# Kernel optimization log

Measured on AMD Instinct MI355X. Metric: run time of the kernel, lower is better.

The kernel has to match this reference:

```python
import jax, jax.numpy as jnp
import numpy as np

DN = ('NCHW', 'OIHW', 'NCHW')

def conv3x3(x, w, b):
    y = jax.lax.conv_general_dilated(x, w, window_strides=(1, 1), padding='SAME', dimension_numbers=DN)
    return y + b[None, :, None, None]

def setup_inputs() -> dict:
    key = jax.random.key(0)
    ks = jax.random.split(key, 12)
    B, C, H, W, r = 4, 64, 128, 128, 2
    ic = C * r * r  # 256
    s = 0.02
    inp = {
        'x': jax.random.normal(ks[0], (B, C, H, W), jnp.float32),
        'g_w': jax.random.normal(ks[1], (ic, ic), jnp.float32) * s,
        'g_b': jnp.zeros((ic,), jnp.float32),
        'theta_w': jax.random.normal(ks[2], (ic, ic), jnp.float32) * s,
        'theta_b': jnp.zeros((ic,), jnp.float32),
        'phi_w': jax.random.normal(ks[3], (ic, ic), jnp.float32) * s,
        'phi_b': jnp.zeros((ic,), jnp.float32),
        'Ws_w': jax.random.normal(ks[4], (C, C), jnp.float32) * s,
        'Ws_b': jnp.zeros((C,), jnp.float32),
        'Wc_w': jax.random.normal(ks[5], (C, C), jnp.float32) * s,
        'Wc_b': jnp.zeros((C,), jnp.float32),
        'gamma_s': jnp.ones((1,), jnp.float32),
        'gamma_c': jnp.ones((1,), jnp.float32),
        'm1_w': jax.random.normal(ks[6], (16, C, 3, 3), jnp.float32) * s,
        'm1_b': jnp.zeros((16,), jnp.float32),
        'm2_w': jax.random.normal(ks[7], (1, 16, 3, 3), jnp.float32) * s,
        'm2_b': jnp.zeros((1,), jnp.float32),
    }
    return inp

def reference(x, g_w, g_b, theta_w, theta_b, phi_w, phi_b, Ws_w, Ws_b, Wc_w, Wc_b, gamma_s, gamma_c, m1_w, m1_b, m2_w, m2_b):
    b, c, h, w = x.shape
    ic = g_w.shape[0]
    r = int(round((ic // c) ** 0.5))
    hr, wr = h // r, w // r
    n = hr * wr  # spatial positions after channel-folding
    # x1: [b, ic, n] (row-major reshape, same as torch .reshape)
    x1 = x.reshape(b, ic, n)
    # 1x1 convs == channel matmuls
    g_x = jnp.einsum('oi,bin->bno', g_w, x1) + g_b          # [b, n, ic]
    th = jnp.einsum('oi,bin->bon', theta_w, x1) + theta_b[:, None]  # [b, ic, n]
    ph = jnp.einsum('oi,bin->bon', phi_w, x1) + phi_b[:, None]      # [b, ic, n]
    # spatial attention: [b, n, n]
    f_s = jnp.einsum('bcn,bcm->bnm', th, ph)
    f_s = jax.nn.softmax(f_s, axis=-1)
    y_s = jnp.einsum('bnm,bmo->bno', f_s, g_x)              # [b, n, ic]
    y_s = jnp.transpose(y_s, (0, 2, 1)).reshape(b, c, h, w)
    # channel attention: [b, ic, ic]
    f_c = jnp.einsum('bcn,bdn->bcd', th, ph)
    f_c = jax.nn.softmax(f_c, axis=-1)
    y_c = jnp.einsum('bno,bod->bnd', g_x, f_c).reshape(b, c, h, w)
    ws = jnp.einsum('oi,bihw->bohw', Ws_w, y_s) + Ws_b[None, :, None, None]
    wc = jnp.einsum('oi,bihw->bohw', Wc_w, y_c) + Wc_b[None, :, None, None]
    z = x + gamma_s[0] * ws + gamma_c[0] * wc
    hmid = jax.nn.relu(conv3x3(z, m1_w, m1_b))
    logit = conv3x3(hmid, m2_w, m2_b)
    return (logit, z)
```

## Files before the change

### kernel.cpp

```cpp
#include <hip/hip_runtime.h>
#include <stdint.h>

typedef unsigned short u16;
typedef unsigned int   u32;

typedef __attribute__((ext_vector_type(8)))  short bf16x8;
typedef __attribute__((ext_vector_type(4)))  float f32x4;

__device__ __forceinline__ float b2f(u16 u) { return __uint_as_float(((u32)u) << 16); }
__device__ __forceinline__ float blo(u32 u) { return __uint_as_float(u << 16); }
__device__ __forceinline__ float bhi(u32 u) { return __uint_as_float(u & 0xffff0000u); }
__device__ __forceinline__ u16 f2b(float f) {
    u32 x = __float_as_uint(f);
    u32 r = (x + 0x7fffu + ((x >> 16) & 1u)) >> 16;
    return (u16)r;
}

#define NB   4
#define IC   256
#define NPOS 4096
#define CH   64
#define HW   16384

__global__ __launch_bounds__(256) void prep_kernel(
    const float* __restrict__ wsw, const float* __restrict__ wcw,
    const float* __restrict__ m1w,
    const float* __restrict__ thw, const float* __restrict__ phw, const float* __restrict__ gw,
    float* __restrict__ wswT, float* __restrict__ wcwT, float* __restrict__ m1wT,
    u16* __restrict__ wbf)
{
    int idx = blockIdx.x * 256 + threadIdx.x;
    if (idx < 65536) {
        wbf[idx]          = f2b(thw[idx]);
        wbf[idx + 65536]  = f2b(phw[idx]);
        wbf[idx + 131072] = f2b(gw[idx]);
    }
    if (idx < 4096) {
        int i = idx >> 6, c = idx & 63;
        wswT[i*64 + c] = wsw[c*64 + i];
        wcwT[i*64 + c] = wcw[c*64 + i];
    }
    if (idx < 9216) {
        int o = idx & 15, ct = idx >> 4;
        int t = ct % 9, c = ct / 9;
        m1wT[idx] = m1w[(o*64 + c)*9 + t];
    }
}

__global__ __launch_bounds__(256) void qkv_mfma_kernel(
    const float* __restrict__ x, const u16* __restrict__ wbf,
    const float* __restrict__ thb, const float* __restrict__ phb, const float* __restrict__ gb,
    u16* __restrict__ Q, u16* __restrict__ K, u16* __restrict__ VT)
{
    __shared__ __align__(16) u32 xT[64*132];
    __shared__ __align__(16) float bias_l[256];
    const int tid  = threadIdx.x;
    const int w    = tid >> 6;
    const int lane = tid & 63;
    const int q4   = lane >> 4;
    const int l    = lane & 15;
    const int n0   = blockIdx.x * 64;
    const int b    = blockIdx.y;
    const int mat  = blockIdx.z;
    const u16* wmat = wbf + mat * 65536;
    const float* bias = (mat == 0) ? thb : (mat == 1) ? phb : gb;

    bias_l[tid] = bias[tid];

    {
        const float* xb = x + ((size_t)b*IC)*NPOS + n0;
        int n   = tid & 63;
        int ip0 = tid >> 6;
        #pragma unroll 4
        for (int p=0; p<32; p++){
            int ip = ip0 + p*4;
            float v0 = xb[(size_t)(2*ip  )*NPOS + n];
            float v1 = xb[(size_t)(2*ip+1)*NPOS + n];
            xT[n*132 + ip] = (u32)f2b(v0) | ((u32)f2b(v1) << 16);
        }
    }
    __syncthreads();

    f32x4 acc[4][4];
    #pragma unroll
    for (int ot=0; ot<4; ot++)
        #pragma unroll
        for (int nt=0; nt<4; nt++) acc[ot][nt] = (f32x4){0.f,0.f,0.f,0.f};

    #pragma unroll
    for (int f=0; f<8; f++){
        bf16x8 bfrag[4];
        #pragma unroll
        for (int nt=0; nt<4; nt++)
            bfrag[nt] = *(const bf16x8*)&xT[(nt*16 + l)*132 + f*16 + q4*4];
        #pragma unroll
        for (int ot=0; ot<4; ot++){
            bf16x8 afrag = *(const bf16x8*)(wmat + (size_t)(w*64 + ot*16 + l)*256 + f*32 + q4*8);
            #pragma unroll
            for (int nt=0; nt<4; nt++)
                acc[ot][nt] = __builtin_amdgcn_mfma_f32_16x16x32_bf16(afrag, bfrag[nt], acc[ot][nt], 0, 0, 0);
        }
    }
    __syncthreads();

    if (mat < 2){
        u16* zbuf = (u16*)xT;
        #pragma unroll
        for (int nt=0; nt<4; nt++)
            #pragma unroll
            for (int ot=0; ot<4; ot++){
                int o = w*64 + ot*16 + q4*4;
                float4 bv = *(const float4*)&bias_l[o];
                uint2 pk;
                pk.x = (u32)f2b(acc[ot][nt][0]+bv.x) | ((u32)f2b(acc[ot][nt][1]+bv.y) << 16);
                pk.y = (u32)f2b(acc[ot][nt][2]+bv.z) | ((u32)f2b(acc[ot][nt][3]+bv.w) << 16);
                *(uint2*)&zbuf[(nt*16 + l)*264 + o] = pk;
            }
        __syncthreads();
        u16* dst = ((mat == 0) ? Q : K) + ((size_t)(b*NPOS + n0))*IC;
        int n = tid >> 2, o0 = (tid & 3)*64;
        const u32* src = &xT[n*132 + (tid & 3)*32];
        #pragma unroll
        for (int m=0; m<8; m++)
            *(uint4*)(dst + (size_t)n*IC + o0 + m*8) = ((const uint4*)src)[m];
    } else {
        u16* zbuf = (u16*)xT;
        #pragma unroll
        for (int nt=0; nt<4; nt++)
            #pragma unroll
            for (int ot=0; ot<4; ot++){
                int o = w*64 + ot*16 + q4*4;
                int n = nt*16 + l;
                #pragma unroll
                for (int reg=0; reg<4; reg++)
                    zbuf[(o+reg)*66 + n] = f2b(acc[ot][nt][reg] + bias_l[o+reg]);
            }
        __syncthreads();
        const u32* src = &xT[tid*33];
        u32 tmp[32];
        #pragma unroll
        for (int m=0; m<32; m++) tmp[m] = src[m];
        u16* dst = VT + ((size_t)(b*IC + tid))*NPOS + n0;
        #pragma unroll
        for (int m=0; m<8; m++){
            uint4 v; v.x = tmp[m*4]; v.y = tmp[m*4+1]; v.z = tmp[m*4+2]; v.w = tmp[m*4+3];
            *(uint4*)(dst + m*8) = v;
        }
    }
}

__global__ __launch_bounds__(256) void fc_mfma_kernel(
    const u16* __restrict__ Q, const u16* __restrict__ K, float* __restrict__ fcp)
{
    __shared__ __align__(16) u16 QT[64*72];
    __shared__ __align__(16) u16 KT[64*72];
    const int tid = threadIdx.x;
    const int w   = tid >> 6;
    const int lane = tid & 63;
    const int q4  = lane >> 4;
    const int l   = lane & 15;
    const int c0  = blockIdx.x * 64;
    const int d0  = blockIdx.y * 64;
    const int b   = blockIdx.z >> 2;
    const int nseg= blockIdx.z & 3;

    f32x4 acc[4];
    #pragma unroll
    for (int dt=0; dt<4; dt++) acc[dt] = (f32x4){0.f,0.f,0.f,0.f};

    for (int chunk=0; chunk<16; chunk++){
        const int n0 = nseg*1024 + chunk*64;
        __syncthreads();
        {
            int r  = tid >> 2;
            int cq = (tid & 3) * 16;
            const u16* qs = Q + ((size_t)(b*NPOS + n0 + r))*IC + c0 + cq;
            const u16* ks = K + ((size_t)(b*NPOS + n0 + r))*IC + d0 + cq;
            u16 qv[16], kv[16];
            *(uint4*)&qv[0] = *(const uint4*)qs;
            *(uint4*)&qv[8] = *(const uint4*)(qs + 8);
            *(uint4*)&kv[0] = *(const uint4*)ks;
            *(uint4*)&kv[8] = *(const uint4*)(ks + 8);
            #pragma unroll
            for (int j=0;j<16;j++){
                QT[(cq+j)*72 + r] = qv[j];
                KT[(cq+j)*72 + r] = kv[j];
            }
        }
        __syncthreads();
        #pragma unroll
        for (int f=0; f<2; f++){
            bf16x8 af = *(const bf16x8*)&QT[(w*16 + l)*72 + f*32 + q4*8];
            #pragma unroll
            for (int dt=0; dt<4; dt++){
                bf16x8 bf2 = *(const bf16x8*)&KT[(dt*16 + l)*72 + f*32 + q4*8];
                acc[dt] = __builtin_amdgcn_mfma_f32_16x16x32_bf16(af, bf2, acc[dt], 0, 0, 0);
            }
        }
    }

    #pragma unroll
    for (int dt=0; dt<4; dt++)
        #pragma unroll
        for (int reg=0; reg<4; reg++)
            fcp[((size_t)((nseg*NB + b)*256 + c0 + w*16 + q4*4 + reg))*256 + d0 + dt*16 + l] = acc[dt][reg];
}

__global__ __launch_bounds__(256) void softmax_fc_kernel(
    const float* __restrict__ fcp, float* __restrict__ pc)
{
    __shared__ float red[8];
    const int tid = threadIdx.x;
    const int b = blockIdx.x >> 8, c = blockIdx.x & 255;
    float v = 0.f;
    #pragma unroll
    for (int s=0; s<4; s++)
        v += fcp[((size_t)((s*NB + b)*256 + c))*256 + tid];
    float m = v;
    #pragma unroll
    for (int d=32; d>=1; d>>=1) m = fmaxf(m, __shfl_xor(m, d));
    if ((tid & 63) == 0) red[tid>>6] = m;
    __syncthreads();
    m = fmaxf(fmaxf(red[0],red[1]), fmaxf(red[2],red[3]));
    float e = __expf(v - m);
    float s = e;
    #pragma unroll
    for (int d=32; d>=1; d>>=1) s += __shfl_xor(s, d);
    if ((tid & 63) == 0) red[4 + (tid>>6)] = s;
    __syncthreads();
    s = red[4]+red[5]+red[6]+red[7];
    pc[(size_t)b*65536 + (size_t)c*256 + tid] = e / s;
}

__global__ __launch_bounds__(256) void yc_kernel(
    const u16* __restrict__ VT, const float* __restrict__ pc, u16* __restrict__ ycb)
{
    __shared__ __align__(16) u16 Vt_l[32*64];
    __shared__ __align__(16) float Pt[32*64];
    const int tid = threadIdx.x;
    const int n0 = blockIdx.x * 64, d0 = blockIdx.y * 64, b = blockIdx.z;
    const int tn = tid >> 4, td = tid & 15;
    float acc[4][4];
    #pragma unroll
    for (int j=0;j<4;j++)
        #pragma unroll
        for (int d=0;d<4;d++) acc[j][d]=0.f;
    for (int ot=0; ot<8; ot++){
        int o0 = ot*32;
        __syncthreads();
        {
            int ol = tid >> 3, cc = tid & 7;
            *(uint4*)&Vt_l[ol*64 + cc*8] = *(const uint4*)(VT + ((size_t)(b*IC + o0 + ol))*NPOS + n0 + cc*8);
            const float* ps = pc + (size_t)b*65536 + (size_t)(o0 + ol)*256 + d0 + cc*8;
            *(float4*)&Pt[ol*64 + cc*8]     = *(const float4*)ps;
            *(float4*)&Pt[ol*64 + cc*8 + 4] = *(const float4*)(ps + 4);
        }
        __syncthreads();
        #pragma unroll 4
        for (int kk=0; kk<32; kk++){
            float4 pv = *(const float4*)&Pt[kk*64 + td*4];
            uint2 vp = *(const uint2*)&Vt_l[kk*64 + tn*4];
            float v0 = blo(vp.x), v1 = bhi(vp.x), v2 = blo(vp.y), v3 = bhi(vp.y);
            acc[0][0] = fmaf(v0, pv.x, acc[0][0]); acc[0][1] = fmaf(v0, pv.y, acc[0][1]);
            acc[0][2] = fmaf(v0, pv.z, acc[0][2]); acc[0][3] = fmaf(v0, pv.w, acc[0][3]);
            acc[1][0] = fmaf(v1, pv.x, acc[1][0]); acc[1][1] = fmaf(v1, pv.y, acc[1][1]);
            acc[1][2] = fmaf(v1, pv.z, acc[1][2]); acc[1][3] = fmaf(v1, pv.w, acc[1][3]);
            acc[2][0] = fmaf(v2, pv.x, acc[2][0]); acc[2][1] = fmaf(v2, pv.y, acc[2][1]);
            acc[2][2] = fmaf(v2, pv.z, acc[2][2]); acc[2][3] = fmaf(v2, pv.w, acc[2][3]);
            acc[3][0] = fmaf(v3, pv.x, acc[3][0]); acc[3][1] = fmaf(v3, pv.y, acc[3][1]);
            acc[3][2] = fmaf(v3, pv.z, acc[3][2]); acc[3][3] = fmaf(v3, pv.w, acc[3][3]);
        }
    }
    #pragma unroll
    for (int j=0;j<4;j++){
        u32 lo = (u32)f2b(acc[j][0]) | ((u32)f2b(acc[j][1]) << 16);
        u32 hi = (u32)f2b(acc[j][2]) | ((u32)f2b(acc[j][3]) << 16);
        *(uint2*)&ycb[((size_t)b*NPOS + n0 + tn*4 + j)*IC + d0 + td*4] = make_uint2(lo,hi);
    }
}

__global__ __launch_bounds__(256) void flash_mfma_kernel(
    const u16* __restrict__ Q, const u16* __restrict__ K, const u16* __restrict__ VT,
    u16* __restrict__ opart0, u16* __restrict__ opartx, float* __restrict__ lpart,
    int sshift)
{
    __shared__ __align__(16) u32 Kt[8192];
    __shared__ __align__(16) u32 Vt[8192];
    __shared__ __align__(16) u16 Pl[4608];
    const int tid  = threadIdx.x;
    const int w    = tid >> 6;
    const int lane = tid & 63;
    const int q4   = lane >> 4;
    const int l    = lane & 15;
    const int S    = 1 << sshift;
    const int b    = blockIdx.y >> sshift;
    const int seg  = blockIdx.y & (S - 1);
    const int n0   = blockIdx.x * 64;
    const int tiles = 64 >> sshift;
    const int kt0   = seg * tiles;

    bf16x8 qf[8];
    {
        const u16* qrow = Q + ((size_t)(b*NPOS + n0 + w*16 + l))*IC;
        #pragma unroll
        for (int f=0; f<8; f++)
            qf[f] = *(const bf16x8*)(qrow + f*32 + q4*8);
    }

    f32x4 oacc[16];
    #pragma unroll
    for (int t=0;t<16;t++) oacc[t] = (f32x4){0.f,0.f,0.f,0.f};
    float lrow[4] = {0.f, 0.f, 0.f, 0.f};

    u16* Pz = Pl + w*1152;

    auto stage_k = [&](int m0s){
        #pragma unroll
        for (int j=0;j<8;j++){
            int call = w*8 + j;
            int r = call*2 + (lane>>5);
            int c = (lane & 31) ^ (r & 7);
            const u16* g = K + ((size_t)(b*NPOS + m0s + r))*IC + c*8;
            __builtin_amdgcn_global_load_lds(
                (const __attribute__((address_space(1))) u32*)(const void*)g,
                (__attribute__((address_space(3))) u32*)(void*)&Kt[call*256], 16, 0, 0);
        }
    };
    auto stage_v = [&](int m0s){
        #pragma unroll
        for (int j=0;j<8;j++){
            int call = w*8 + j;
            int d = call*8 + (lane>>3);
            int c = (lane & 7) ^ (d & 7);
            const u16* g = VT + ((size_t)(b*IC + d))*NPOS + m0s + c*8;
            __builtin_amdgcn_global_load_lds(
                (const __attribute__((address_space(1))) u32*)(const void*)g,
                (__attribute__((address_space(3))) u32*)(void*)&Vt[call*256], 16, 0, 0);
        }
    };

    stage_k(kt0*64);
    stage_v(kt0*64);
    asm volatile("s_waitcnt vmcnt(0)" ::: "memory");
    __builtin_amdgcn_sched_barrier(0);
    __builtin_amdgcn_s_barrier();
    __builtin_amdgcn_sched_barrier(0);

    for (int kti=0; kti<tiles; kti++){
        const bool more = (kti + 1 < tiles);
        const int mn = (kt0 + kti + 1)*64;

        f32x4 sac[4];
        #pragma unroll
        for (int t=0;t<4;t++) sac[t] = (f32x4){0.f,0.f,0.f,0.f};
        __builtin_amdgcn_s_setprio(1);
        #pragma unroll
        for (int f=0; f<8; f++){
            #pragma unroll
            for (int t=0;t<4;t++){
                int r = t*16 + l;
                int c = (f*4 + q4) ^ (r & 7);
                bf16x8 kf = *(const bf16x8*)((const u16*)Kt + r*256 + c*8);
                sac[t] = __builtin_amdgcn_mfma_f32_16x16x32_bf16(qf[f], kf, sac[t], 0, 0, 0);
            }
        }
        __builtin_amdgcn_s_setprio(0);

        __builtin_amdgcn_sched_barrier(0);
        __builtin_amdgcn_s_barrier();
        __builtin_amdgcn_sched_barrier(0);

        if (more) stage_k(mn);

        #pragma unroll
        for (int reg=0; reg<4; reg++){
            float p0 = __expf(sac[0][reg]), p1 = __expf(sac[1][reg]);
            float p2 = __expf(sac[2][reg]), p3 = __expf(sac[3][reg]);
            lrow[reg] += (p0+p1) + (p2+p3);
            int m = q4*4 + reg;
            Pz[m*72 + l]      = f2b(p0);
            Pz[m*72 + 16 + l] = f2b(p1);
            Pz[m*72 + 32 + l] = f2b(p2);
            Pz[m*72 + 48 + l] = f2b(p3);
        }

        if (more) { asm volatile("s_waitcnt vmcnt(8)" ::: "memory"); }
        else      { asm volatile("s_waitcnt vmcnt(0)" ::: "memory"); }
        __builtin_amdgcn_sched_barrier(0);
        __builtin_amdgcn_s_barrier();
        __builtin_amdgcn_sched_barrier(0);

        __builtin_amdgcn_s_setprio(1);
        #pragma unroll
        for (int s2=0; s2<2; s2++){
            bf16x8 pa = *(const bf16x8*)(Pz + l*72 + s2*32 + q4*8);
            #pragma unroll
            for (int t=0;t<16;t++){
                int d = t*16 + l;
                int c = (s2*4 + q4) ^ (d & 7);
                bf16x8 vb = *(const bf16x8*)((const u16*)Vt + d*64 + c*8);
                oacc[t] = __builtin_amdgcn_mfma_f32_16x16x32_bf16(pa, vb, oacc[t], 0, 0, 0);
            }
        }
        __builtin_amdgcn_s_setprio(0);

        __builtin_amdgcn_sched_barrier(0);
        __builtin_amdgcn_s_barrier();
        __builtin_amdgcn_sched_barrier(0);

        if (more) {
            stage_v(mn);
            asm volatile("s_waitcnt vmcnt(8)" ::: "memory");
        } else {
            asm volatile("s_waitcnt vmcnt(0)" ::: "memory");
        }
        __builtin_amdgcn_sched_barrier(0);
        __builtin_amdgcn_s_barrier();
        __builtin_amdgcn_sched_barrier(0);
    }

    #pragma unroll
    for (int reg=0; reg<4; reg++){
        float v = lrow[reg];
        v += __shfl_xor(v, 1); v += __shfl_xor(v, 2);
        v += __shfl_xor(v, 4); v += __shfl_xor(v, 8);
        if (l == 0)
            lpart[((size_t)(seg*NB + b))*NPOS + n0 + w*16 + q4*4 + reg] = v;
    }

    __syncthreads();
    u16* Ez = (u16*)Kt + w*4096;
    #pragma unroll
    for (int t=0;t<16;t++)
        #pragma unroll
        for (int reg=0;reg<4;reg++)
            Ez[(t*16 + l)*16 + q4*4 + reg] = f2b(oacc[t][reg]);
    u16* base = (seg == 0) ? opart0 : (opartx + (size_t)(seg-1)*((size_t)NB*IC*NPOS));
    u16* dst = base + (size_t)b*(IC*NPOS) + n0 + w*16;
    for (int p=0; p<32; p++){
        int d = p*8 + (lane>>3);
        u32 val = *(const u32*)(Ez + d*16 + (lane&7)*2);
        *(u32*)(dst + (size_t)d*NPOS + (lane&7)*2) = val;
    }
}

__global__ __launch_bounds__(256) void combine_kernel(
    u16* __restrict__ opart0, const u16* __restrict__ opartx,
    const float* __restrict__ lpart, int S)
{
    const int idx = blockIdx.x * 256 + threadIdx.x;
    const int b   = idx >> 17;
    const int rem = idx & 131071;
    const int o   = rem >> 9;
    const int n   = (rem & 511) * 8;
    const size_t base = ((size_t)b*IC + o)*NPOS + n;
    float acc[8] = {0,0,0,0,0,0,0,0};
    float L[8]   = {0,0,0,0,0,0,0,0};
    for (int s=0; s<S; s++){
        const u16* p = (s == 0) ? opart0 : (opartx + (size_t)(s-1)*((size_t)NB*IC*NPOS));
        uint4 v = *(const uint4*)(p + base);
        acc[0] += blo(v.x); acc[1] += bhi(v.x);
        acc[2] += blo(v.y); acc[3] += bhi(v.y);
        acc[4] += blo(v.z); acc[5] += bhi(v.z);
        acc[6] += blo(v.w); acc[7] += bhi(v.w);
        const float* lp = lpart + ((size_t)(s*NB + b))*NPOS + n;
        float4 l0 = *(const float4*)lp;
        float4 l1 = *(const float4*)(lp + 4);
        L[0]+=l0.x; L[1]+=l0.y; L[2]+=l0.z; L[3]+=l0.w;
        L[4]+=l1.x; L[5]+=l1.y; L[6]+=l1.z; L[7]+=l1.w;
    }
    uint4 out;
    out.x = (u32)f2b(acc[0]/L[0]) | ((u32)f2b(acc[1]/L[1]) << 16);
    out.y = (u32)f2b(acc[2]/L[2]) | ((u32)f2b(acc[3]/L[3]) << 16);
    out.z = (u32)f2b(acc[4]/L[4]) | ((u32)f2b(acc[5]/L[5]) << 16);
    out.w = (u32)f2b(acc[6]/L[6]) | ((u32)f2b(acc[7]/L[7]) << 16);
    *(uint4*)(opart0 + base) = out;
}

__global__ __launch_bounds__(256) void z_kernel(
    const float* __restrict__ x, const u16* __restrict__ ysT, const u16* __restrict__ ycb,
    const float* __restrict__ wswT, const float* __restrict__ wcwT,
    const float* __restrict__ wsb, const float* __restrict__ wcb,
    const float* __restrict__ gs, const float* __restrict__ gc,
    float* __restrict__ zout)
{
    __shared__ __align__(16) float Wsl[64*32];
    __shared__ __align__(16) float Wcl[64*32];
    const int tid = threadIdx.x;
    const int p = blockIdx.x * 256 + tid;
    const int cbase = blockIdx.y * 32;
    const int b = blockIdx.z;
    {
        int i = tid >> 2, c8 = (tid & 3) * 8;
        const float* s1 = wswT + i*64 + cbase + c8;
        const float* s2 = wcwT + i*64 + cbase + c8;
        *(float4*)&Wsl[i*32 + c8]     = *(const float4*)s1;
        *(float4*)&Wsl[i*32 + c8 + 4] = *(const float4*)(s1+4);
        *(float4*)&Wcl[i*32 + c8]     = *(const float4*)s2;
        *(float4*)&Wcl[i*32 + c8 + 4] = *(const float4*)(s2+4);
    }
    __syncthreads();
    float as[32], ac[32];
    #pragma unroll
    for (int c=0;c<32;c++){ as[c]=0.f; ac[c]=0.f; }
    const u16* ysp = ysT + (size_t)b*(IC*NPOS) + p;
    const u16* ycp = ycb + (size_t)b*(IC*NPOS) + p;
    for (int i=0;i<64;i++){
        float ysv = b2f(ysp[(size_t)i*HW]);
        float ycv = b2f(ycp[(size_t)i*HW]);
        #pragma unroll
        for (int c=0;c<32;c++){
            as[c] = fmaf(Wsl[i*32+c], ysv, as[c]);
            ac[c] = fmaf(Wcl[i*32+c], ycv, ac[c]);
        }
    }
    float gsv = gs[0], gcv = gc[0];
    #pragma unroll
    for (int c=0;c<32;c++){
        int cg = cbase + c;
        float xv = x[((size_t)b*CH + cg)*HW + p];
        float zv = fmaf(gsv, as[c] + wsb[cg], xv);
        zv = fmaf(gcv, ac[c] + wcb[cg], zv);
        zout[((size_t)b*CH + cg)*HW + p] = zv;
    }
}

__global__ __launch_bounds__(256) void conv1_kernel(
    const float* __restrict__ z, const float* __restrict__ m1wT, const float* __restrict__ m1b,
    float* __restrict__ hmid)
{
    const int tid = threadIdx.x;
    const int p = blockIdx.x * 128 + (tid & 127);
    const int oh = (tid >> 7) * 8;
    const int b = blockIdx.y;
    const int y = p >> 7, xx = p & 127;
    float acc[8];
    #pragma unroll
    for (int o=0;o<8;o++) acc[o]=0.f;
    for (int c=0;c<64;c++){
        const float* zp = z + ((size_t)b*CH + c)*HW;
        #pragma unroll
        for (int t=0;t<9;t++){
            int dy = t/3 - 1, dx = t%3 - 1;
            int yy = y + dy, xv = xx + dx;
            float zv = 0.f;
            if (yy >= 0 && yy < 128 && xv >= 0 && xv < 128) zv = zp[yy*128 + xv];
            const float* w = m1wT + (c*9 + t)*16 + oh;
            #pragma unroll
            for (int o=0;o<8;o++) acc[o] = fmaf(w[o], zv, acc[o]);
        }
    }
    #pragma unroll
    for (int o=0;o<8;o++)
        hmid[((size_t)b*16 + oh + o)*HW + p] = fmaxf(acc[o] + m1b[oh + o], 0.f);
}

__global__ __launch_bounds__(256) void conv2_kernel(
    const float* __restrict__ hmid, const float* __restrict__ m2w, const float* __restrict__ m2b,
    float* __restrict__ logit)
{
    const int idx = blockIdx.x * 256 + threadIdx.x;
    const int b = idx >> 14, p = idx & 16383;
    const int y = p >> 7, xx = p & 127;
    float acc = 0.f;
    for (int c=0;c<16;c++){
        const float* hp = hmid + ((size_t)b*16 + c)*HW;
        #pragma unroll
        for (int t=0;t<9;t++){
            int dy = t/3 - 1, dx = t%3 - 1;
            int yy = y + dy, xv = xx + dx;
            if (yy >= 0 && yy < 128 && xv >= 0 && xv < 128)
                acc = fmaf(m2w[c*9+t], hp[yy*128 + xv], acc);
        }
    }
    logit[idx] = acc + m2b[0];
}

extern "C" void kernel_launch(void* const* d_in, const int* in_sizes, int n_in,
                              void* d_out, int out_size, void* d_ws, size_t ws_size,
                              hipStream_t stream)
{
    const float* x    = (const float*)d_in[0];
    const float* g_w  = (const float*)d_in[1];
    const float* g_b  = (const float*)d_in[2];
    const float* th_w = (const float*)d_in[3];
    const float* th_b = (const float*)d_in[4];
    const float* ph_w = (const float*)d_in[5];
    const float* ph_b = (const float*)d_in[6];
    const float* ws_w = (const float*)d_in[7];
    const float* ws_b = (const float*)d_in[8];
    const float* wc_w = (const float*)d_in[9];
    const float* wc_b = (const float*)d_in[10];
    const float* gs   = (const float*)d_in[11];
    const float* gc   = (const float*)d_in[12];
    const float* m1w  = (const float*)d_in[13];
    const float* m1b  = (const float*)d_in[14];
    const float* m2w  = (const float*)d_in[15];
    const float* m2b  = (const float*)d_in[16];

    char* ws = (char*)d_ws;
    u16*   Qb   = (u16*)  (ws + 0);
    u16*   Kb   = (u16*)  (ws + 8388608);
    u16*   VTb  = (u16*)  (ws + 16777216);
    u16*   ysT  = (u16*)  (ws + 25165824);
    u16*   ycb  = (u16*)  (ws + 33554432);
    u16*   wbf  = (u16*)  (ws + 41943040);
    float* pc   = (float*)(ws + 42991616);
    float* fcp  = (float*)(ws + 44040192);
    float* hmid = (float*)(ws + 44040192);
    float* lpart= (float*)(ws + 44040192);
    float* wswT = (float*)(ws + 48234496);
    float* wcwT = (float*)(ws + 48250880);
    float* m1wT = (float*)(ws + 48267264);
    u16*   opartx = (u16*)(ws + 48304128);

    float* logit = (float*)d_out;
    float* zout  = (float*)d_out + 65536;

    int sshift = 0;
    if (ws_size >= 48304128ULL + 3ULL*8388608ULL)      sshift = 2;
    else if (ws_size >= 48304128ULL + 1ULL*8388608ULL) sshift = 1;

    prep_kernel<<<256, 256, 0, stream>>>(ws_w, wc_w, m1w, th_w, ph_w, g_w,
                                         wswT, wcwT, m1wT, wbf);
    qkv_mfma_kernel<<<dim3(64,4,3), 256, 0, stream>>>(x, wbf, th_b, ph_b, g_b, Qb, Kb, VTb);
    fc_mfma_kernel<<<dim3(4,4,16), 256, 0, stream>>>(Qb, Kb, fcp);
    softmax_fc_kernel<<<1024, 256, 0, stream>>>(fcp, pc);
    yc_kernel<<<dim3(64,4,4), 256, 0, stream>>>(VTb, pc, ycb);
    flash_mfma_kernel<<<dim3(64, NB << sshift), 256, 0, stream>>>(Qb, Kb, VTb, ysT, opartx, lpart, sshift);
    combine_kernel<<<2048, 256, 0, stream>>>(ysT, opartx, lpart, 1 << sshift);
    z_kernel<<<dim3(64,2,4), 256, 0, stream>>>(x, ysT, ycb, wswT, wcwT, ws_b, wc_b, gs, gc, zout);
    conv1_kernel<<<dim3(128,4), 256, 0, stream>>>(zout, m1wT, m1b, hmid);
    conv2_kernel<<<256, 256, 0, stream>>>(hmid, m2w, m2b, logit);
}
```

Before: 459.4 us.

## Switch flash attention kernel to 32x32x16 MFMA with 2x2 wave tiling

Restructures the flash attention kernel to use 32x32x16 bf16 MFMA instructions. The four waves now form a 2x2 grid over query rows and key columns instead of each wave owning 16 query rows across all keys. Each wave computes its partial QK^T split across two accumulators, writes exponentials into a shared swizzled P tile, and computes a quarter of the output channels. The row-sum reduction across the key halves goes through LDS. It also sets launch_bounds to 2 blocks per CU. The aim is fewer, larger MFMAs and fewer LDS fragment reads per FLOP, at the cost of more register pressure and an extra cross-wave sum.

```diff
diff --git a/kernel.cpp b/kernel.cpp
--- a/kernel.cpp
+++ b/kernel.cpp
@@ -6,6 +6,7 @@
 
 typedef __attribute__((ext_vector_type(8)))  short bf16x8;
 typedef __attribute__((ext_vector_type(4)))  float f32x4;
+typedef __attribute__((ext_vector_type(16))) float f32x16;
 
 __device__ __forceinline__ float b2f(u16 u) { return __uint_as_float(((u32)u) << 16); }
 __device__ __forceinline__ float blo(u32 u) { return __uint_as_float(u << 16); }
@@ -279,40 +280,45 @@
     }
 }
 
-__global__ __launch_bounds__(256) void flash_mfma_kernel(
+__global__ __launch_bounds__(256, 2) void flash_mfma_kernel(
     const u16* __restrict__ Q, const u16* __restrict__ K, const u16* __restrict__ VT,
     u16* __restrict__ opart0, u16* __restrict__ opartx, float* __restrict__ lpart,
     int sshift)
 {
     __shared__ __align__(16) u32 Kt[8192];
     __shared__ __align__(16) u32 Vt[8192];
-    __shared__ __align__(16) u16 Pl[4608];
+    __shared__ __align__(16) u16 Pl[4096];
     const int tid  = threadIdx.x;
     const int w    = tid >> 6;
     const int lane = tid & 63;
-    const int q4   = lane >> 4;
-    const int l    = lane & 15;
+    const int l31  = lane & 31;
+    const int hi   = lane >> 5;
+    const int wq   = w >> 1;
+    const int wk   = w & 1;
     const int S    = 1 << sshift;
     const int b    = blockIdx.y >> sshift;
     const int seg  = blockIdx.y & (S - 1);
     const int n0   = blockIdx.x * 64;
     const int tiles = 64 >> sshift;
     const int kt0   = seg * tiles;
-
-    bf16x8 qf[8];
+    const int sw    = l31 & 7;
+
+    bf16x8 qf[16];
     {
-        const u16* qrow = Q + ((size_t)(b*NPOS + n0 + w*16 + l))*IC;
-        #pragma unroll
-        for (int f=0; f<8; f++)
-            qf[f] = *(const bf16x8*)(qrow + f*32 + q4*8);
-    }
-
-    f32x4 oacc[16];
-    #pragma unroll
-    for (int t=0;t<16;t++) oacc[t] = (f32x4){0.f,0.f,0.f,0.f};
-    float lrow[4] = {0.f, 0.f, 0.f, 0.f};
-
-    u16* Pz = Pl + w*1152;
+        const u16* qrow = Q + ((size_t)(b*NPOS + n0 + wq*32 + l31))*IC;
+        #pragma unroll
+        for (int st=0; st<16; st++)
+            qf[st] = *(const bf16x8*)(qrow + st*16 + hi*8);
+    }
+
+    f32x16 oacc[4];
+    #pragma unroll
+    for (int t=0;t<4;t++)
+        #pragma unroll
+        for (int i=0;i<16;i++) oacc[t][i] = 0.f;
+    float lsum[16];
+    #pragma unroll
+    for (int i=0;i<16;i++) lsum[i] = 0.f;
 
     auto stage_k = [&](int m0s){
         #pragma unroll
@@ -346,60 +352,56 @@
     __builtin_amdgcn_s_barrier();
     __builtin_amdgcn_sched_barrier(0);
 
+    const u16* KtRow = (const u16*)Kt + (wk*32 + l31)*256;
+    const u16* PlRow = Pl + (wq*32 + l31)*64;
+    const u16* VtW   = (const u16*)Vt + (wk*128 + l31)*64;
+
     for (int kti=0; kti<tiles; kti++){
         const bool more = (kti + 1 < tiles);
         const int mn = (kt0 + kti + 1)*64;
 
-        f32x4 sac[4];
-        #pragma unroll
-        for (int t=0;t<4;t++) sac[t] = (f32x4){0.f,0.f,0.f,0.f};
+        f32x16 sA, sB;
+        #pragma unroll
+        for (int i=0;i<16;i++){ sA[i]=0.f; sB[i]=0.f; }
         __builtin_amdgcn_s_setprio(1);
         #pragma unroll
-        for (int f=0; f<8; f++){
+        for (int st=0; st<8; st++){
+            bf16x8 ka = *(const bf16x8*)(KtRow + ((st*2+hi) ^ sw)*8);
+            sA = __builtin_amdgcn_mfma_f32_32x32x16_bf16(qf[st], ka, sA, 0, 0, 0);
+            bf16x8 kb = *(const bf16x8*)(KtRow + (((st+8)*2+hi) ^ sw)*8);
+            sB = __builtin_amdgcn_mfma_f32_32x32x16_bf16(qf[st+8], kb, sB, 0, 0, 0);
+        }
+        __builtin_amdgcn_s_setprio(0);
+
+        #pragma unroll
+        for (int reg=0; reg<16; reg++){
+            float p = __expf(sA[reg] + sB[reg]);
+            lsum[reg] += p;
+            int q = wq*32 + (reg&3) + 8*(reg>>2) + 4*hi;
+            int cpos = (((wk*4 + (l31>>3)) ^ (q&7)) * 8) + (lane & 7);
+            Pl[q*64 + cpos] = f2b(p);
+        }
+
+        __builtin_amdgcn_sched_barrier(0);
+        __builtin_amdgcn_s_barrier();
+        __builtin_amdgcn_sched_barrier(0);
+
+        if (more) stage_k(mn);
+
+        if (more) { asm volatile("s_waitcnt vmcnt(8) lgkmcnt(0)" ::: "memory"); }
+        else      { asm volatile("s_waitcnt vmcnt(0) lgkmcnt(0)" ::: "memory"); }
+        __builtin_amdgcn_sched_barrier(0);
+        __builtin_amdgcn_s_barrier();
+        __builtin_amdgcn_sched_barrier(0);
+
+        __builtin_amdgcn_s_setprio(1);
+        #pragma unroll
+        for (int ks=0; ks<4; ks++){
+            bf16x8 pa = *(const bf16x8*)(PlRow + ((ks*2+hi) ^ sw)*8);
             #pragma unroll
-            for (int t=0;t<4;t++){
-                int r = t*16 + l;
-                int c = (f*4 + q4) ^ (r & 7);
-                bf16x8 kf = *(const bf16x8*)((const u16*)Kt + r*256 + c*8);
-                sac[t] = __builtin_amdgcn_mfma_f32_16x16x32_bf16(qf[f], kf, sac[t], 0, 0, 0);
-            }
-        }
-        __builtin_amdgcn_s_setprio(0);
-
-        __builtin_amdgcn_sched_barrier(0);
-        __builtin_amdgcn_s_barrier();
-        __builtin_amdgcn_sched_barrier(0);
-
-        if (more) stage_k(mn);
-
-        #pragma unroll
-        for (int reg=0; reg<4; reg++){
-            float p0 = __expf(sac[0][reg]), p1 = __expf(sac[1][reg]);
-            float p2 = __expf(sac[2][reg]), p3 = __expf(sac[3][reg]);
-            lrow[reg] += (p0+p1) + (p2+p3);
-            int m = q4*4 + reg;
-            Pz[m*72 + l]      = f2b(p0);
-            Pz[m*72 + 16 + l] = f2b(p1);
-            Pz[m*72 + 32 + l] = f2b(p2);
-            Pz[m*72 + 48 + l] = f2b(p3);
-        }
-
-        if (more) { asm volatile("s_waitcnt vmcnt(8)" ::: "memory"); }
-        else      { asm volatile("s_waitcnt vmcnt(0)" ::: "memory"); }
-        __builtin_amdgcn_sched_barrier(0);
-        __builtin_amdgcn_s_barrier();
-        __builtin_amdgcn_sched_barrier(0);
-
-        __builtin_amdgcn_s_setprio(1);
-        #pragma unroll
-        for (int s2=0; s2<2; s2++){
-            bf16x8 pa = *(const bf16x8*)(Pz + l*72 + s2*32 + q4*8);
-            #pragma unroll
-            for (int t=0;t<16;t++){
-                int d = t*16 + l;
-                int c = (s2*4 + q4) ^ (d & 7);
-                bf16x8 vb = *(const bf16x8*)((const u16*)Vt + d*64 + c*8);
-                oacc[t] = __builtin_amdgcn_mfma_f32_16x16x32_bf16(pa, vb, oacc[t], 0, 0, 0);
+            for (int dt=0; dt<4; dt++){
+                bf16x8 vb = *(const bf16x8*)(VtW + dt*2048 + ((ks*2+hi) ^ sw)*8);
+                oacc[dt] = __builtin_amdgcn_mfma_f32_32x32x16_bf16(pa, vb, oacc[dt], 0, 0, 0);
             }
         }
         __builtin_amdgcn_s_setprio(0);
@@ -419,28 +421,52 @@
         __builtin_amdgcn_sched_barrier(0);
     }
 
-    #pragma unroll
-    for (int reg=0; reg<4; reg++){
-        float v = lrow[reg];
-        v += __shfl_xor(v, 1); v += __shfl_xor(v, 2);
-        v += __shfl_xor(v, 4); v += __shfl_xor(v, 8);
-        if (l == 0)
-            lpart[((size_t)(seg*NB + b))*NPOS + n0 + w*16 + q4*4 + reg] = v;
-    }
-
+    float lv[16];
+    #pragma unroll
+    for (int reg=0; reg<16; reg++){
+        float v = lsum[reg];
+        v += __shfl_xor(v, 1); v += __shfl_xor(v, 2); v += __shfl_xor(v, 4);
+        v += __shfl_xor(v, 8); v += __shfl_xor(v, 16);
+        lv[reg] = v;
+    }
+    float* lred = (float*)Pl;
+    if (wk == 1 && l31 == 0){
+        #pragma unroll
+        for (int reg=0; reg<16; reg++)
+            lred[wq*32 + (reg&3) + 8*(reg>>2) + 4*hi] = lv[reg];
+    }
+
+    u16* LDSO = (u16*)Kt;
+    #pragma unroll
+    for (int dt=0; dt<4; dt++){
+        int d = wk*128 + dt*32 + l31;
+        int dsw = d & 15;
+        #pragma unroll
+        for (int pr=0; pr<8; pr++){
+            int r0 = pr*2;
+            int n = wq*32 + (r0&3) + 8*(r0>>2) + 4*hi;
+            u32 pk = (u32)f2b(oacc[dt][r0]) | ((u32)f2b(oacc[dt][r0+1]) << 16);
+            *(u32*)&LDSO[d*64 + (((n>>1) ^ dsw) * 2)] = pk;
+        }
+    }
     __syncthreads();
-    u16* Ez = (u16*)Kt + w*4096;
-    #pragma unroll
-    for (int t=0;t<16;t++)
-        #pragma unroll
-        for (int reg=0;reg<4;reg++)
-            Ez[(t*16 + l)*16 + q4*4 + reg] = f2b(oacc[t][reg]);
-    u16* base = (seg == 0) ? opart0 : (opartx + (size_t)(seg-1)*((size_t)NB*IC*NPOS));
-    u16* dst = base + (size_t)b*(IC*NPOS) + n0 + w*16;
+
+    if (wk == 0 && l31 == 0){
+        #pragma unroll
+        for (int reg=0; reg<16; reg++){
+            int row = wq*32 + (reg&3) + 8*(reg>>2) + 4*hi;
+            lpart[((size_t)(seg*NB + b))*NPOS + n0 + row] = lv[reg] + lred[row];
+        }
+    }
+
+    u16* basep = (seg == 0) ? opart0 : (opartx + (size_t)(seg-1)*((size_t)NB*IC*NPOS));
+    u16* dst = basep + (size_t)b*(IC*NPOS) + n0;
+    #pragma unroll 4
     for (int p=0; p<32; p++){
-        int d = p*8 + (lane>>3);
-        u32 val = *(const u32*)(Ez + d*16 + (lane&7)*2);
-        *(u32*)(dst + (size_t)d*NPOS + (lane&7)*2) = val;
+        int d = w*64 + p*2 + hi;
+        int n2 = l31*2;
+        u32 val = *(const u32*)&LDSO[d*64 + (((n2>>1) ^ (d & 15)) * 2)];
+        *(u32*)(dst + (size_t)d*NPOS + n2) = val;
     }
 }
 
```

Result: slower. 477.1 us (+3.9%).

## Widen flash attention blocks to 8 waves sharing K/V tiles with XCD-aware mapping

Applied to the files above, without the earlier changes.

The flash attention kernel now runs 512 threads (8 waves) per block covering 128 query rows, so each staged K/V tile in LDS is reused by twice as many waves and each wave issues half as many global-to-LDS loads. Block indices are remapped so that consecutive blocks assigned to the same XCD work on the same batch, which should improve L2 locality for K and V. The P scratch buffer switches from padded rows to an XOR-swizzled layout to save LDS while avoiding bank conflicts. The cost is fewer blocks in the grid and higher per-block LDS and register pressure, which could reduce occupancy.

```diff
diff --git a/kernel.cpp b/kernel.cpp
--- a/kernel.cpp
+++ b/kernel.cpp
@@ -279,23 +279,28 @@
     }
 }
 
-__global__ __launch_bounds__(256) void flash_mfma_kernel(
+__global__ __launch_bounds__(512, 4) void flash_mfma_kernel(
     const u16* __restrict__ Q, const u16* __restrict__ K, const u16* __restrict__ VT,
     u16* __restrict__ opart0, u16* __restrict__ opartx, float* __restrict__ lpart,
     int sshift)
 {
-    __shared__ __align__(16) u32 Kt[8192];
-    __shared__ __align__(16) u32 Vt[8192];
-    __shared__ __align__(16) u16 Pl[4608];
+    __shared__ __align__(16) u32 lds[20480];
+    u32* Kt = lds;
+    u32* Vt = lds + 8192;
+    u16* Pl = (u16*)(lds + 16384);
     const int tid  = threadIdx.x;
     const int w    = tid >> 6;
     const int lane = tid & 63;
     const int q4   = lane >> 4;
     const int l    = lane & 15;
     const int S    = 1 << sshift;
-    const int b    = blockIdx.y >> sshift;
-    const int seg  = blockIdx.y & (S - 1);
-    const int n0   = blockIdx.x * 64;
+
+    const int id   = blockIdx.x;
+    const int xcd  = id & 7;
+    const int r    = id >> 3;
+    const int b    = xcd >> 1;
+    const int seg  = r & (S - 1);
+    const int n0   = ((r >> sshift) | ((xcd & 1) << 4)) << 7;
     const int tiles = 64 >> sshift;
     const int kt0   = seg * tiles;
 
@@ -312,15 +317,15 @@
     for (int t=0;t<16;t++) oacc[t] = (f32x4){0.f,0.f,0.f,0.f};
     float lrow[4] = {0.f, 0.f, 0.f, 0.f};
 
-    u16* Pz = Pl + w*1152;
+    u16* Pz = Pl + w*1024;
 
     auto stage_k = [&](int m0s){
         #pragma unroll
-        for (int j=0;j<8;j++){
-            int call = w*8 + j;
-            int r = call*2 + (lane>>5);
-            int c = (lane & 31) ^ (r & 7);
-            const u16* g = K + ((size_t)(b*NPOS + m0s + r))*IC + c*8;
+        for (int j=0;j<4;j++){
+            int call = w*4 + j;
+            int rr = call*2 + (lane>>5);
+            int c = (lane & 31) ^ (rr & 7);
+            const u16* g = K + ((size_t)(b*NPOS + m0s + rr))*IC + c*8;
             __builtin_amdgcn_global_load_lds(
                 (const __attribute__((address_space(1))) u32*)(const void*)g,
                 (__attribute__((address_space(3))) u32*)(void*)&Kt[call*256], 16, 0, 0);
@@ -328,8 +333,8 @@
     };
     auto stage_v = [&](int m0s){
         #pragma unroll
-        for (int j=0;j<8;j++){
-            int call = w*8 + j;
+        for (int j=0;j<4;j++){
+            int call = w*4 + j;
             int d = call*8 + (lane>>3);
             int c = (lane & 7) ^ (d & 7);
             const u16* g = VT + ((size_t)(b*IC + d))*NPOS + m0s + c*8;
@@ -358,9 +363,9 @@
         for (int f=0; f<8; f++){
             #pragma unroll
             for (int t=0;t<4;t++){
-                int r = t*16 + l;
-                int c = (f*4 + q4) ^ (r & 7);
-                bf16x8 kf = *(const bf16x8*)((const u16*)Kt + r*256 + c*8);
+                int rr = t*16 + l;
+                int c = (f*4 + q4) ^ (rr & 7);
+                bf16x8 kf = *(const bf16x8*)((const u16*)Kt + rr*256 + c*8);
                 sac[t] = __builtin_amdgcn_mfma_f32_16x16x32_bf16(qf[f], kf, sac[t], 0, 0, 0);
             }
         }
@@ -378,13 +383,14 @@
             float p2 = __expf(sac[2][reg]), p3 = __expf(sac[3][reg]);
             lrow[reg] += (p0+p1) + (p2+p3);
             int m = q4*4 + reg;
-            Pz[m*72 + l]      = f2b(p0);
-            Pz[m*72 + 16 + l] = f2b(p1);
-            Pz[m*72 + 32 + l] = f2b(p2);
-            Pz[m*72 + 48 + l] = f2b(p3);
-        }
-
-        if (more) { asm volatile("s_waitcnt vmcnt(8)" ::: "memory"); }
+            int j = l & 7, hb = l >> 3;
+            Pz[m*64 + (((0*2+hb) ^ (m&7))*8) + j] = f2b(p0);
+            Pz[m*64 + (((1*2+hb) ^ (m&7))*8) + j] = f2b(p1);
+            Pz[m*64 + (((2*2+hb) ^ (m&7))*8) + j] = f2b(p2);
+            Pz[m*64 + (((3*2+hb) ^ (m&7))*8) + j] = f2b(p3);
+        }
+
+        if (more) { asm volatile("s_waitcnt vmcnt(4)" ::: "memory"); }
         else      { asm volatile("s_waitcnt vmcnt(0)" ::: "memory"); }
         __builtin_amdgcn_sched_barrier(0);
         __builtin_amdgcn_s_barrier();
@@ -393,7 +399,7 @@
         __builtin_amdgcn_s_setprio(1);
         #pragma unroll
         for (int s2=0; s2<2; s2++){
-            bf16x8 pa = *(const bf16x8*)(Pz + l*72 + s2*32 + q4*8);
+            bf16x8 pa = *(const bf16x8*)(Pz + l*64 + (((s2*4 + q4) ^ (l&7))*8));
             #pragma unroll
             for (int t=0;t<16;t++){
                 int d = t*16 + l;
@@ -410,7 +416,7 @@
 
         if (more) {
             stage_v(mn);
-            asm volatile("s_waitcnt vmcnt(8)" ::: "memory");
+            asm volatile("s_waitcnt vmcnt(4)" ::: "memory");
         } else {
             asm volatile("s_waitcnt vmcnt(0)" ::: "memory");
         }
@@ -429,7 +435,7 @@
     }
 
     __syncthreads();
-    u16* Ez = (u16*)Kt + w*4096;
+    u16* Ez = (u16*)lds + w*4096;
     #pragma unroll
     for (int t=0;t<16;t++)
         #pragma unroll
@@ -627,7 +633,7 @@
     fc_mfma_kernel<<<dim3(4,4,16), 256, 0, stream>>>(Qb, Kb, fcp);
     softmax_fc_kernel<<<1024, 256, 0, stream>>>(fcp, pc);
     yc_kernel<<<dim3(64,4,4), 256, 0, stream>>>(VTb, pc, ycb);
-    flash_mfma_kernel<<<dim3(64, NB << sshift), 256, 0, stream>>>(Qb, Kb, VTb, ysT, opartx, lpart, sshift);
+    flash_mfma_kernel<<<dim3(32 * (NB << sshift)), 512, 0, stream>>>(Qb, Kb, VTb, ysT, opartx, lpart, sshift);
     combine_kernel<<<2048, 256, 0, stream>>>(ysT, opartx, lpart, 1 << sshift);
     z_kernel<<<dim3(64,2,4), 256, 0, stream>>>(x, ysT, ycb, wswT, wcwT, ws_b, wc_b, gs, gc, zout);
     conv1_kernel<<<dim3(128,4), 256, 0, stream>>>(zout, m1wT, m1b, hmid);
```

After: 605.1 us. 31.7% more time.
